# Kernel tuning notes

Measured on AMD Instinct MI355X. Metric: run time of the kernel, lower is better.

Reference implementation:

```python
import jax, jax.numpy as jnp
import numpy as np

N_HEAD = 16
D_MODEL = 1024
D_HEAD = 64
SCALE = 1.0 / D_HEAD ** 0.5
LN_EPS = 1e-5


def layer_norm(x, g, b):
    mu = jnp.mean(x, axis=-1, keepdims=True)
    var = jnp.mean(jnp.square(x - mu), axis=-1, keepdims=True)
    return (x - mu) * jax.lax.rsqrt(var + LN_EPS) * g + b


def setup_inputs() -> dict:
    key = jax.random.key(0)
    ks = jax.random.split(key, 6)
    T, B = 2048, 4
    h = jax.random.normal(ks[0], (T, B, D_MODEL), dtype=jnp.float32)
    # key-padding mask, shape (klen, bsz); True = masked
    attn_mask = jax.random.randint(ks[1], (T, B), 0, 2).astype(jnp.bool_)
    s = 1.0 / np.sqrt(D_MODEL)
    wq = jax.random.uniform(ks[2], (N_HEAD * D_HEAD, D_MODEL), minval=-s, maxval=s, dtype=jnp.float32)
    wkv = jax.random.uniform(ks[3], (2 * N_HEAD * D_HEAD, D_MODEL), minval=-s, maxval=s, dtype=jnp.float32)
    wo = jax.random.uniform(ks[4], (D_MODEL, N_HEAD * D_HEAD), minval=-s, maxval=s, dtype=jnp.float32)
    ln_g = jnp.ones((D_MODEL,), jnp.float32)
    ln_b = jnp.zeros((D_MODEL,), jnp.float32)
    return {"h": h, "attn_mask": attn_mask, "wq": wq, "wkv": wkv,
            "wo": wo, "ln_g": ln_g, "ln_b": ln_b}


def reference(h, attn_mask, wq, wkv, wo, ln_g, ln_b):
    T, B, _ = h.shape
    c = h  # mems is None
    head_q = (h @ wq.T).reshape(T, B, N_HEAD, D_HEAD)
    kv = c @ wkv.T
    head_k, head_v = jnp.split(kv, 2, axis=-1)
    head_k = head_k.reshape(T, B, N_HEAD, D_HEAD)
    head_v = head_v.reshape(T, B, N_HEAD, D_HEAD)

    # scores: [qlen, klen, bsz, n_head]
    attn_score = jnp.einsum('ibnd,jbnd->ijbn', head_q, head_k) * SCALE
    attn_score = jnp.where(attn_mask[None, :, :, None], -jnp.inf, attn_score)
    attn_prob = jax.nn.softmax(attn_score, axis=1)

    attn_vec = jnp.einsum('ijbn,jbnd->ibnd', attn_prob, head_v)
    attn_vec = attn_vec.reshape(T, B, N_HEAD * D_HEAD)
    attn_out = attn_vec @ wo.T
    # post-lnorm residual (pre_lnorm=False); gate='plus' path unused here
    return layer_norm(h + attn_out, ln_g, ln_b)
```

## Files before the change

kernel.cpp:

```cpp
#include <hip/hip_runtime.h>

#define T_LEN 2048
#define BSZ 4
#define NHEAD 16
#define DHEAD 64
#define DMODEL 1024
#define SCALE 0.125f
#define L2E_SCALE (0.125f * 1.44269504f)

typedef __bf16 bf16x8 __attribute__((ext_vector_type(8)));
typedef float f32x4 __attribute__((ext_vector_type(4)));

__device__ __forceinline__ float bf2f(unsigned short u) {
  union { unsigned int i; float f; } v; v.i = ((unsigned int)u) << 16; return v.f;
}
__device__ __forceinline__ unsigned short f2bf(float f) {
  union { float f; unsigned int i; } v; v.f = f;
  unsigned int r = v.i + 0x7fffu + ((v.i >> 16) & 1u);
  return (unsigned short)(r >> 16);
}

typedef __attribute__((address_space(1))) void* gptr_t;
typedef __attribute__((address_space(3))) void* lptr_t;

__device__ __forceinline__ void load_lds16(const void* g, void* l) {
  __builtin_amdgcn_global_load_lds((gptr_t)g, (lptr_t)l, 16, 0, 0);
}

__device__ __forceinline__ int swz16(int row, int g) {
  return row * 64 + ((g ^ (row & 7)) << 3);
}

__global__ __launch_bounds__(256) void cvt_prep(const float* __restrict__ h,
                                                const float* __restrict__ wq,
                                                const float* __restrict__ wkv,
                                                const float* __restrict__ wo,
                                                const unsigned char* __restrict__ mask,
                                                unsigned short* __restrict__ h_bf,
                                                unsigned short* __restrict__ wq_bf,
                                                unsigned short* __restrict__ wkv_bf,
                                                unsigned short* __restrict__ wo_bf,
                                                int* __restrict__ pos,
                                                int* __restrict__ nkeys) {
  const int tid = threadIdx.x;
  if (blockIdx.x < 12288) {
    const size_t E4 = (size_t)T_LEN * BSZ * DMODEL / 4;
    const size_t W4 = (size_t)NHEAD * DHEAD * DMODEL / 4;
    const size_t g = (size_t)blockIdx.x * 256 + tid;
    const float* src; unsigned short* dst; size_t off;
    if (g < E4)                { src = h;   dst = h_bf;   off = g; }
    else if (g < E4 + W4)      { src = wq;  dst = wq_bf;  off = g - E4; }
    else if (g < E4 + 3 * W4)  { src = wkv; dst = wkv_bf; off = g - E4 - W4; }
    else                       { src = wo;  dst = wo_bf;  off = g - E4 - 3 * W4; }
    const float4 v = *(const float4*)(src + off * 4);
    ushort4 o;
    o.x = f2bf(v.x); o.y = f2bf(v.y); o.z = f2bf(v.z); o.w = f2bf(v.w);
    *(ushort4*)(dst + off * 4) = o;
    return;
  }
  __shared__ int s_any;
  if (tid == 0) s_any = 0;
  __syncthreads();
  int acc = 0;
  for (int i = tid; i < T_LEN * BSZ; i += 256)
    if ((i & 3) != 0 && mask[i] != 0) acc = 1;
  if (acc) atomicOr(&s_any, 1);
  __syncthreads();
  const int mmode = s_any ? 0 : 1;
  const int wv = tid >> 6, lane = tid & 63;
  const int b = wv;
  int run = 0;
  for (int j0 = 0; j0 < T_LEN; j0 += 64) {
    const int j = j0 + lane;
    const int mval = mmode ? ((const int*)mask)[(size_t)j * BSZ + b]
                           : (int)mask[(size_t)j * BSZ + b];
    const int keep = (mval == 0) ? 1 : 0;
    int x = keep;
#pragma unroll
    for (int off = 1; off < 64; off <<= 1) {
      const int y = __shfl_up(x, off, 64);
      if (lane >= off) x += y;
    }
    pos[b * T_LEN + j] = keep ? (run + x - keep) : -1;
    run += __shfl(x, 63, 64);
  }
  if (lane == 0) nkeys[b] = run;
}

#define GEMM64_DBUF(Aptr, Bptr)                                                        \
  const int tid  = threadIdx.x;                                                        \
  const int lane = tid & 63;                                                           \
  const int wv   = tid >> 6;                                                           \
  const int wr = (wv >> 1) * 64;                                                       \
  const int wc = (wv & 1) * 64;                                                        \
  const int mi   = lane & 15;                                                          \
  const int quad = lane >> 4;                                                          \
  f32x4 acc[4][4] = {};                                                                \
  int rowc[4], colc[4];                                                                \
  _Pragma("unroll")                                                                    \
  for (int c = 0; c < 4; c++) {                                                        \
    const int s = c * 256 + tid;                                                       \
    rowc[c] = s >> 3;                                                                  \
    colc[c] = ((s & 7) ^ (rowc[c] & 7)) * 8;                                           \
  }                                                                                    \
  const int swz = mi & 7;                                                              \
  _Pragma("unroll")                                                                    \
  for (int c = 0; c < 4; c++) {                                                        \
    load_lds16(Aptr + (size_t)rowc[c] * DMODEL + colc[c], As + c * 2048 + wv * 512);   \
    load_lds16(Bptr + (size_t)rowc[c] * DMODEL + colc[c], Bs + c * 2048 + wv * 512);   \
  }                                                                                    \
  for (int k0 = 0; k0 < DMODEL; k0 += 64) {                                            \
    const int cur = (k0 >> 6) & 1;                                                     \
    const unsigned short* Asr = As + cur * 8192;                                       \
    const unsigned short* Bsr = Bs + cur * 8192;                                       \
    unsigned short* Asw = As + (1 - cur) * 8192;                                       \
    unsigned short* Bsw = Bs + (1 - cur) * 8192;                                       \
    __syncthreads();                                                                   \
    if (k0 + 64 < DMODEL) {                                                            \
      _Pragma("unroll")                                                                \
      for (int c = 0; c < 4; c++) {                                                    \
        load_lds16(Aptr + (size_t)rowc[c] * DMODEL + k0 + 64 + colc[c], Asw + c * 2048 + wv * 512); \
        load_lds16(Bptr + (size_t)rowc[c] * DMODEL + k0 + 64 + colc[c], Bsw + c * 2048 + wv * 512); \
      }                                                                                \
    }                                                                                  \
    _Pragma("unroll")                                                                  \
    for (int kq = 0; kq < 2; kq++) {                                                   \
      const int cp = ((kq * 4 + quad) ^ swz) * 8;                                      \
      bf16x8 af[4], bfr[4];                                                            \
      _Pragma("unroll")                                                                \
      for (int rt = 0; rt < 4; rt++)                                                   \
        af[rt] = *(const bf16x8*)(Asr + (wr + rt * 16 + mi) * 64 + cp);                \
      _Pragma("unroll")                                                                \
      for (int ct = 0; ct < 4; ct++)                                                   \
        bfr[ct] = *(const bf16x8*)(Bsr + (wc + ct * 16 + mi) * 64 + cp);               \
      _Pragma("unroll")                                                                \
      for (int rt = 0; rt < 4; rt++)                                                   \
        _Pragma("unroll")                                                              \
        for (int ct = 0; ct < 4; ct++)                                                 \
          acc[rt][ct] = __builtin_amdgcn_mfma_f32_16x16x32_bf16(af[rt], bfr[ct], acc[rt][ct], 0, 0, 0); \
    }                                                                                  \
  }

__global__ __launch_bounds__(256) void gemm_qkv(const unsigned short* __restrict__ A,
                                                const unsigned short* __restrict__ Wq,
                                                const unsigned short* __restrict__ Wkv,
                                                const int* __restrict__ pos,
                                                unsigned short* __restrict__ outQ,
                                                unsigned short* __restrict__ outK,
                                                unsigned short* __restrict__ outVt) {
  __shared__ alignas(16) unsigned short As[2 * 128 * 64];
  __shared__ alignas(16) unsigned short Bs[2 * 128 * 64];
  const int m0 = blockIdx.y * 128;
  const int n0 = blockIdx.x * 128;
  const unsigned short* Abase = A + (size_t)m0 * DMODEL;
  const unsigned short* Bbase = (n0 < DMODEL) ? (Wq + (size_t)n0 * DMODEL)
                                              : (Wkv + (size_t)(n0 - DMODEL) * DMODEL);
  GEMM64_DBUF(Abase, Bbase)

  const int region = n0 >> 10;
#pragma unroll
  for (int rt = 0; rt < 4; rt++) {
#pragma unroll
    for (int r = 0; r < 4; r++) {
      const int gm = m0 + wr + rt * 16 + quad * 4 + r;
      const int i = gm >> 2, b = gm & 3;
      int p = i;
      if (region > 0) p = pos[b * T_LEN + i];
      if (region > 0 && p < 0) continue;
#pragma unroll
      for (int ct = 0; ct < 4; ct++) {
        const int gn = n0 + wc + ct * 16 + mi;
        const int gnl = gn & (DMODEL - 1);
        const int hn = gnl >> 6, d = gnl & 63;
        const float v = acc[rt][ct][r];
        if (region == 0)
          outQ[(((size_t)b * NHEAD + hn) * T_LEN + i) * DHEAD + d] = f2bf(v * L2E_SCALE);
        else if (region == 1)
          outK[(((size_t)b * NHEAD + hn) * T_LEN + p) * DHEAD + d] = f2bf(v);
        else
          outVt[(((size_t)b * NHEAD + hn) * DHEAD + d) * T_LEN + p] = f2bf(v);
      }
    }
  }
}

__global__ __launch_bounds__(256) void gemm_out(const unsigned short* __restrict__ A,
                                                const unsigned short* __restrict__ Bw,
                                                unsigned short* __restrict__ outB) {
  __shared__ alignas(16) unsigned short As[2 * 128 * 64];
  __shared__ alignas(16) unsigned short Bs[2 * 128 * 64];
  const int m0 = blockIdx.y * 128;
  const int n0 = blockIdx.x * 128;
  const unsigned short* Abase = A  + (size_t)m0 * DMODEL;
  const unsigned short* Bbase = Bw + (size_t)n0 * DMODEL;
  GEMM64_DBUF(Abase, Bbase)

#pragma unroll
  for (int rt = 0; rt < 4; rt++)
#pragma unroll
    for (int ct = 0; ct < 4; ct++)
#pragma unroll
      for (int r = 0; r < 4; r++) {
        const int gm = m0 + wr + rt * 16 + quad * 4 + r;
        const int gn = n0 + wc + ct * 16 + mi;
        outB[(size_t)gm * DMODEL + gn] = f2bf(acc[rt][ct][r]);
      }
}

template<bool TAIL>
__device__ __forceinline__ void attn_chunk(int j0, int nk, int mi, int quad,
    const unsigned short* Ks, const unsigned short* Vts, unsigned short* PsW,
    const bf16x8 (&qb)[2][2], f32x4 (&oc)[2][4], float (&rs)[2]) {
  f32x4 sc[2][4] = {};
  __builtin_amdgcn_s_setprio(1);
#pragma unroll
  for (int ct = 0; ct < 4; ct++) {
    const bf16x8 kf0 = *(const bf16x8*)(Ks + swz16(ct * 16 + mi, quad));
    const bf16x8 kf1 = *(const bf16x8*)(Ks + swz16(ct * 16 + mi, 4 + quad));
#pragma unroll
    for (int g = 0; g < 2; g++) {
      sc[g][ct] = __builtin_amdgcn_mfma_f32_16x16x32_bf16(kf0, qb[g][0], sc[g][ct], 0, 0, 0);
      sc[g][ct] = __builtin_amdgcn_mfma_f32_16x16x32_bf16(kf1, qb[g][1], sc[g][ct], 0, 0, 0);
    }
  }
  __builtin_amdgcn_s_setprio(0);
#pragma unroll
  for (int g = 0; g < 2; g++)
#pragma unroll
    for (int ct = 0; ct < 4; ct++) {
#pragma unroll
      for (int r = 0; r < 4; r++) {
        float p = __builtin_amdgcn_exp2f(sc[g][ct][r]);
        if (TAIL && (j0 + ct * 16 + quad * 4 + r >= nk)) p = 0.f;
        rs[g] += p;
        sc[g][ct][r] = p;
      }
      union { float f; unsigned u; } c0, c1, c2, c3;
      c0.f = sc[g][ct][0]; c1.f = sc[g][ct][1]; c2.f = sc[g][ct][2]; c3.f = sc[g][ct][3];
      const unsigned pk0 = (c0.u >> 16) | (c1.u & 0xFFFF0000u);
      const unsigned pk1 = (c2.u >> 16) | (c3.u & 0xFFFF0000u);
      const int prow = g * 16 + mi;
      *(uint2*)(PsW + prow * 64 + (((2 * ct + (quad >> 1)) ^ (prow & 7)) << 3)
                + (quad & 1) * 4) = make_uint2(pk0, pk1);
    }
  bf16x8 pa0[2], pa1[2];
#pragma unroll
  for (int g = 0; g < 2; g++) {
    pa0[g] = *(const bf16x8*)(PsW + swz16(g * 16 + mi, quad));
    pa1[g] = *(const bf16x8*)(PsW + swz16(g * 16 + mi, 4 + quad));
  }
  __builtin_amdgcn_s_setprio(1);
#pragma unroll
  for (int ct = 0; ct < 4; ct++) {
    const bf16x8 vf0 = *(const bf16x8*)(Vts + swz16(ct * 16 + mi, quad));
    const bf16x8 vf1 = *(const bf16x8*)(Vts + swz16(ct * 16 + mi, 4 + quad));
#pragma unroll
    for (int g = 0; g < 2; g++) {
      oc[g][ct] = __builtin_amdgcn_mfma_f32_16x16x32_bf16(pa0[g], vf0, oc[g][ct], 0, 0, 0);
      oc[g][ct] = __builtin_amdgcn_mfma_f32_16x16x32_bf16(pa1[g], vf1, oc[g][ct], 0, 0, 0);
    }
  }
  __builtin_amdgcn_s_setprio(0);
}

__device__ __forceinline__ void stage_kv(const unsigned short* __restrict__ Kg,
                                         const unsigned short* __restrict__ Vtg,
                                         size_t base, int j0s, unsigned short* kb,
                                         int tid, int wv) {
#pragma unroll
  for (int u = 0; u < 2; u++) {
    const int gi = u * 256 + tid;
    const int r = gi >> 3;
    const int gs = (gi ^ r) & 7;
    load_lds16(Kg + base + (size_t)(j0s + r) * DHEAD + gs * 8,
               kb + u * 2048 + wv * 512);
    load_lds16(Vtg + base + (size_t)r * T_LEN + j0s + gs * 8,
               kb + 4096 + u * 2048 + wv * 512);
  }
}

__global__ __launch_bounds__(256, 3) void attn_mfma(const unsigned short* __restrict__ Qg,
                                                    const unsigned short* __restrict__ Kg,
                                                    const unsigned short* __restrict__ Vtg,
                                                    const int* __restrict__ nkeys,
                                                    unsigned short* __restrict__ av) {
  __shared__ alignas(16) unsigned short smem[24832];
  unsigned short* Qs = smem + 16384;
  float* Ls = (float*)(smem + 24576);

  const int tid  = threadIdx.x;
  const int lane = tid & 63;
  const int wv   = tid >> 6;
  const int mi   = lane & 15;
  const int quad = lane >> 4;
  const int bid = blockIdx.x;
  const int p   = ((bid >> 7) << 3) | (bid & 7);
  const int i0  = ((bid >> 3) & 15) * 128;
  const int b   = p >> 4;
  const int n   = p & 15;
  const size_t base = ((size_t)b * NHEAD + n) * T_LEN * DHEAD;
  const int nk = nkeys[b];
  const int nc = (nk + 63) >> 6;

  for (int it = tid; it < 1024; it += 256) {
    const int r = it >> 3, g = it & 7;
    *(uint4*)(Qs + swz16(r, g)) = *(const uint4*)(Qg + base + (size_t)(i0 + r) * DHEAD + g * 8);
  }
  if (nc > 0) stage_kv(Kg, Vtg, base, 0, smem, tid, wv);
  __syncthreads();
  bf16x8 qb[2][2];
#pragma unroll
  for (int g = 0; g < 2; g++) {
    qb[g][0] = *(const bf16x8*)(Qs + swz16(wv * 32 + g * 16 + mi, quad));
    qb[g][1] = *(const bf16x8*)(Qs + swz16(wv * 32 + g * 16 + mi, 4 + quad));
  }

  f32x4 oc[2][4] = {};
  float rs[2] = {0.f, 0.f};
  unsigned short* PsW = Qs + wv * 2048;

  for (int c = 0; c < nc; ++c) {
    if (c + 1 < nc) stage_kv(Kg, Vtg, base, (c + 1) * 64, smem + ((c + 1) & 1) * 8192, tid, wv);
    const unsigned short* Kl = smem + (c & 1) * 8192;
    const unsigned short* Vl = Kl + 4096;
    if (c == nc - 1 && (nk & 63))
      attn_chunk<true>(c * 64, nk, mi, quad, Kl, Vl, PsW, qb, oc, rs);
    else
      attn_chunk<false>(c * 64, nk, mi, quad, Kl, Vl, PsW, qb, oc, rs);
    __syncthreads();
  }

#pragma unroll
  for (int g = 0; g < 2; g++) {
    float t = rs[g];
    t += __shfl_xor(t, 16, 64);
    t += __shfl_xor(t, 32, 64);
    rs[g] = t;
  }
  if (quad == 0) { Ls[wv * 32 + mi] = rs[0]; Ls[wv * 32 + 16 + mi] = rs[1]; }
  __syncthreads();
  float linv[2][4];
#pragma unroll
  for (int g = 0; g < 2; g++)
#pragma unroll
    for (int r = 0; r < 4; r++) {
      const float l = Ls[wv * 32 + g * 16 + quad * 4 + r];
      linv[g][r] = (l > 0.f) ? (1.f / l) : 0.f;
    }
#pragma unroll
  for (int g = 0; g < 2; g++)
#pragma unroll
    for (int ct = 0; ct < 4; ct++)
#pragma unroll
      for (int r = 0; r < 4; r++) {
        const int q = i0 + wv * 32 + g * 16 + quad * 4 + r;
        const int d = ct * 16 + mi;
        av[((size_t)q * BSZ + b) * DMODEL + n * DHEAD + d] = f2bf(oc[g][ct][r] * linv[g][r]);
      }
}

__global__ __launch_bounds__(256) void ln_kernel(const float* __restrict__ h,
                                                 const unsigned short* __restrict__ ao,
                                                 const float* __restrict__ g,
                                                 const float* __restrict__ bb,
                                                 float* __restrict__ out) {
  const int tid = threadIdx.x, lane = tid & 63, wv = tid >> 6;
  const int row = blockIdx.x * 4 + wv;
  const size_t base = (size_t)row * DMODEL;
  float x[16];
  float s = 0.f, sq = 0.f;
#pragma unroll
  for (int k = 0; k < 4; k++) {
    const int c = lane * 4 + k * 256;
    const float4 hv = *(const float4*)(h + base + c);
    const ushort4 a4 = *(const ushort4*)(ao + base + c);
    x[k * 4 + 0] = hv.x + bf2f(a4.x);
    x[k * 4 + 1] = hv.y + bf2f(a4.y);
    x[k * 4 + 2] = hv.z + bf2f(a4.z);
    x[k * 4 + 3] = hv.w + bf2f(a4.w);
#pragma unroll
    for (int j = 0; j < 4; j++) { s += x[k * 4 + j]; sq += x[k * 4 + j] * x[k * 4 + j]; }
  }
#pragma unroll
  for (int off = 32; off; off >>= 1) { s += __shfl_xor(s, off, 64); sq += __shfl_xor(sq, off, 64); }
  const float mu  = s * (1.f / DMODEL);
  const float var = sq * (1.f / DMODEL) - mu * mu;
  const float inv = rsqrtf(var + 1e-5f);
#pragma unroll
  for (int k = 0; k < 4; k++) {
    const int c = lane * 4 + k * 256;
    const float4 gv = *(const float4*)(g + c);
    const float4 bv = *(const float4*)(bb + c);
    float4 o;
    o.x = (x[k * 4 + 0] - mu) * inv * gv.x + bv.x;
    o.y = (x[k * 4 + 1] - mu) * inv * gv.y + bv.y;
    o.z = (x[k * 4 + 2] - mu) * inv * gv.z + bv.z;
    o.w = (x[k * 4 + 3] - mu) * inv * gv.w + bv.w;
    *(float4*)(out + base + c) = o;
  }
}

extern "C" void kernel_launch(void* const* d_in, const int* in_sizes, int n_in,
                              void* d_out, int out_size, void* d_ws, size_t ws_size,
                              hipStream_t stream) {
  (void)in_sizes; (void)n_in; (void)out_size; (void)ws_size;
  const float* h           = (const float*)d_in[0];
  const unsigned char* msk = (const unsigned char*)d_in[1];
  const float* wq          = (const float*)d_in[2];
  const float* wkv         = (const float*)d_in[3];
  const float* wo          = (const float*)d_in[4];
  const float* lng         = (const float*)d_in[5];
  const float* lnb         = (const float*)d_in[6];
  float* out = (float*)d_out;

  const size_t E  = (size_t)T_LEN * BSZ * DMODEL;
  const size_t WQ = (size_t)NHEAD * DHEAD * DMODEL;
  char* ws = (char*)d_ws;
  int* nkeys            = (int*)ws;                       ws += 16;
  int* pos              = (int*)ws;                       ws += (size_t)BSZ * T_LEN * 4;
  unsigned short* h_bf  = (unsigned short*)ws;            ws += E * 2;
  unsigned short* wq_bf = (unsigned short*)ws;            ws += WQ * 2;
  unsigned short* wkv_bf= (unsigned short*)ws;            ws += 2 * WQ * 2;
  unsigned short* wo_bf = (unsigned short*)ws;            ws += WQ * 2;
  unsigned short* Qb    = (unsigned short*)ws;            ws += E * 2;
  unsigned short* Kb    = (unsigned short*)ws;            ws += E * 2;
  unsigned short* Vtb   = (unsigned short*)ws;            ws += E * 2;
  unsigned short* AV    = (unsigned short*)ws;            ws += E * 2;
  unsigned short* AO    = (unsigned short*)ws;

  const dim3 blk(256);
  cvt_prep<<<dim3(12289), blk, 0, stream>>>(h, wq, wkv, wo, msk,
                                            h_bf, wq_bf, wkv_bf, wo_bf, pos, nkeys);
  gemm_qkv<<<dim3(3 * DMODEL / 128, T_LEN * BSZ / 128), blk, 0, stream>>>(
      h_bf, wq_bf, wkv_bf, pos, Qb, Kb, Vtb);
  attn_mfma<<<dim3(1024), blk, 0, stream>>>(Qb, Kb, Vtb, nkeys, AV);
  gemm_out<<<dim3(DMODEL / 128, T_LEN * BSZ / 128), blk, 0, stream>>>(AV, wo_bf, AO);
  ln_kernel<<<dim3(T_LEN * BSZ / 4), blk, 0, stream>>>(h, AO, lng, lnb, out);
}
```

Baseline: 309.6 us.

## Process two 128-query tiles per attention block to reuse staged K/V

Each attention workgroup now handles 256 query rows (two 128-row tiles held in registers) instead of 128. Every K/V chunk staged into LDS is therefore used twice, halving global K/V traffic and staging overhead, and the grid shrinks from 1024 to 512 blocks. The cost is double the accumulator registers per thread, which may reduce occupancy under launch_bounds(256,3), and fewer blocks to spread across CUs. The Ls buffer is enlarged to hold row sums for both tiles.

```diff
diff --git a/kernel.cpp b/kernel.cpp
--- a/kernel.cpp
+++ b/kernel.cpp
@@ -284,7 +284,7 @@
                                                     const unsigned short* __restrict__ Vtg,
                                                     const int* __restrict__ nkeys,
                                                     unsigned short* __restrict__ av) {
-  __shared__ alignas(16) unsigned short smem[24832];
+  __shared__ alignas(16) unsigned short smem[25088];
   unsigned short* Qs = smem + 16384;
   float* Ls = (float*)(smem + 24576);
 
@@ -294,69 +294,83 @@
   const int mi   = lane & 15;
   const int quad = lane >> 4;
   const int bid = blockIdx.x;
-  const int p   = ((bid >> 7) << 3) | (bid & 7);
-  const int i0  = ((bid >> 3) & 15) * 128;
+  const int p   = ((bid >> 6) << 3) | (bid & 7);
+  const int i0  = ((bid >> 3) & 7) * 256;
   const int b   = p >> 4;
   const int n   = p & 15;
   const size_t base = ((size_t)b * NHEAD + n) * T_LEN * DHEAD;
   const int nk = nkeys[b];
   const int nc = (nk + 63) >> 6;
 
-  for (int it = tid; it < 1024; it += 256) {
-    const int r = it >> 3, g = it & 7;
-    *(uint4*)(Qs + swz16(r, g)) = *(const uint4*)(Qg + base + (size_t)(i0 + r) * DHEAD + g * 8);
-  }
   if (nc > 0) stage_kv(Kg, Vtg, base, 0, smem, tid, wv);
-  __syncthreads();
-  bf16x8 qb[2][2];
-#pragma unroll
-  for (int g = 0; g < 2; g++) {
-    qb[g][0] = *(const bf16x8*)(Qs + swz16(wv * 32 + g * 16 + mi, quad));
-    qb[g][1] = *(const bf16x8*)(Qs + swz16(wv * 32 + g * 16 + mi, 4 + quad));
-  }
-
-  f32x4 oc[2][4] = {};
-  float rs[2] = {0.f, 0.f};
+
+  bf16x8 qbA[2][2], qbB[2][2];
+#pragma unroll
+  for (int t = 0; t < 2; t++) {
+    for (int it = tid; it < 1024; it += 256) {
+      const int r = it >> 3, g = it & 7;
+      *(uint4*)(Qs + swz16(r, g)) =
+          *(const uint4*)(Qg + base + (size_t)(i0 + t * 128 + r) * DHEAD + g * 8);
+    }
+    __syncthreads();
+#pragma unroll
+    for (int g = 0; g < 2; g++) {
+      bf16x8 q0 = *(const bf16x8*)(Qs + swz16(wv * 32 + g * 16 + mi, quad));
+      bf16x8 q1 = *(const bf16x8*)(Qs + swz16(wv * 32 + g * 16 + mi, 4 + quad));
+      if (t == 0) { qbA[g][0] = q0; qbA[g][1] = q1; }
+      else        { qbB[g][0] = q0; qbB[g][1] = q1; }
+    }
+    __syncthreads();
+  }
+
+  f32x4 ocA[2][4] = {}, ocB[2][4] = {};
+  float rsA[2] = {0.f, 0.f}, rsB[2] = {0.f, 0.f};
   unsigned short* PsW = Qs + wv * 2048;
 
   for (int c = 0; c < nc; ++c) {
     if (c + 1 < nc) stage_kv(Kg, Vtg, base, (c + 1) * 64, smem + ((c + 1) & 1) * 8192, tid, wv);
     const unsigned short* Kl = smem + (c & 1) * 8192;
     const unsigned short* Vl = Kl + 4096;
-    if (c == nc - 1 && (nk & 63))
-      attn_chunk<true>(c * 64, nk, mi, quad, Kl, Vl, PsW, qb, oc, rs);
-    else
-      attn_chunk<false>(c * 64, nk, mi, quad, Kl, Vl, PsW, qb, oc, rs);
+    const int j0 = c * 64;
+    if (c == nc - 1 && (nk & 63)) {
+      attn_chunk<true>(j0, nk, mi, quad, Kl, Vl, PsW, qbA, ocA, rsA);
+      attn_chunk<true>(j0, nk, mi, quad, Kl, Vl, PsW, qbB, ocB, rsB);
+    } else {
+      attn_chunk<false>(j0, nk, mi, quad, Kl, Vl, PsW, qbA, ocA, rsA);
+      attn_chunk<false>(j0, nk, mi, quad, Kl, Vl, PsW, qbB, ocB, rsB);
+    }
     __syncthreads();
   }
 
 #pragma unroll
   for (int g = 0; g < 2; g++) {
-    float t = rs[g];
-    t += __shfl_xor(t, 16, 64);
-    t += __shfl_xor(t, 32, 64);
-    rs[g] = t;
-  }
-  if (quad == 0) { Ls[wv * 32 + mi] = rs[0]; Ls[wv * 32 + 16 + mi] = rs[1]; }
+    float tA = rsA[g], tB = rsB[g];
+    tA += __shfl_xor(tA, 16, 64); tA += __shfl_xor(tA, 32, 64);
+    tB += __shfl_xor(tB, 16, 64); tB += __shfl_xor(tB, 32, 64);
+    rsA[g] = tA; rsB[g] = tB;
+  }
+  if (quad == 0) {
+    Ls[wv * 32 + mi]        = rsA[0];  Ls[wv * 32 + 16 + mi]       = rsA[1];
+    Ls[128 + wv * 32 + mi]  = rsB[0];  Ls[128 + wv * 32 + 16 + mi] = rsB[1];
+  }
   __syncthreads();
-  float linv[2][4];
-#pragma unroll
-  for (int g = 0; g < 2; g++)
-#pragma unroll
-    for (int r = 0; r < 4; r++) {
-      const float l = Ls[wv * 32 + g * 16 + quad * 4 + r];
-      linv[g][r] = (l > 0.f) ? (1.f / l) : 0.f;
-    }
-#pragma unroll
-  for (int g = 0; g < 2; g++)
-#pragma unroll
-    for (int ct = 0; ct < 4; ct++)
+#pragma unroll
+  for (int t = 0; t < 2; t++) {
+    const f32x4 (&oc)[2][4] = t ? ocB : ocA;
+#pragma unroll
+    for (int g = 0; g < 2; g++)
 #pragma unroll
       for (int r = 0; r < 4; r++) {
-        const int q = i0 + wv * 32 + g * 16 + quad * 4 + r;
-        const int d = ct * 16 + mi;
-        av[((size_t)q * BSZ + b) * DMODEL + n * DHEAD + d] = f2bf(oc[g][ct][r] * linv[g][r]);
+        const float l = Ls[t * 128 + wv * 32 + g * 16 + quad * 4 + r];
+        const float linv = (l > 0.f) ? (1.f / l) : 0.f;
+#pragma unroll
+        for (int ct = 0; ct < 4; ct++) {
+          const int q = i0 + t * 128 + wv * 32 + g * 16 + quad * 4 + r;
+          const int d = ct * 16 + mi;
+          av[((size_t)q * BSZ + b) * DMODEL + n * DHEAD + d] = f2bf(oc[g][ct][r] * linv);
+        }
       }
+  }
 }
 
 __global__ __launch_bounds__(256) void ln_kernel(const float* __restrict__ h,
@@ -433,7 +447,7 @@
                                             h_bf, wq_bf, wkv_bf, wo_bf, pos, nkeys);
   gemm_qkv<<<dim3(3 * DMODEL / 128, T_LEN * BSZ / 128), blk, 0, stream>>>(
       h_bf, wq_bf, wkv_bf, pos, Qb, Kb, Vtb);
-  attn_mfma<<<dim3(1024), blk, 0, stream>>>(Qb, Kb, Vtb, nkeys, AV);
+  attn_mfma<<<dim3(512), blk, 0, stream>>>(Qb, Kb, Vtb, nkeys, AV);
   gemm_out<<<dim3(DMODEL / 128, T_LEN * BSZ / 128), blk, 0, stream>>>(AV, wo_bf, AO);
   ln_kernel<<<dim3(T_LEN * BSZ / 4), blk, 0, stream>>>(h, AO, lng, lnb, out);
 }
```

Result: slower. 414.5 us (+33.9%).

## Read V fragments directly from global memory and drop Q/V LDS staging

Applied to the files above, without the earlier changes.

The attention kernel no longer stages V tiles into shared memory. Each wave now loads its V MFMA fragments straight from global memory inside the PV loop, and Q fragments are loaded directly into registers instead of going through an LDS tile. This cuts LDS use so the launch bound can be raised from 3 to 4 blocks per SM for higher occupancy. The cost is that V is no longer shared across waves and is read from global/L2 on every chunk, and these loads are no longer prefetched asynchronously, so latency may appear in the MFMA loop.

```diff
diff --git a/kernel.cpp b/kernel.cpp
--- a/kernel.cpp
+++ b/kernel.cpp
@@ -209,7 +209,8 @@
 
 template<bool TAIL>
 __device__ __forceinline__ void attn_chunk(int j0, int nk, int mi, int quad,
-    const unsigned short* Ks, const unsigned short* Vts, unsigned short* PsW,
+    const unsigned short* Ks, const unsigned short* __restrict__ Vg,
+    unsigned short* PsW,
     const bf16x8 (&qb)[2][2], f32x4 (&oc)[2][4], float (&rs)[2]) {
   f32x4 sc[2][4] = {};
   __builtin_amdgcn_s_setprio(1);
@@ -252,8 +253,8 @@
   __builtin_amdgcn_s_setprio(1);
 #pragma unroll
   for (int ct = 0; ct < 4; ct++) {
-    const bf16x8 vf0 = *(const bf16x8*)(Vts + swz16(ct * 16 + mi, quad));
-    const bf16x8 vf1 = *(const bf16x8*)(Vts + swz16(ct * 16 + mi, 4 + quad));
+    const bf16x8 vf0 = *(const bf16x8*)(Vg + (size_t)(ct * 16 + mi) * T_LEN + j0 + quad * 8);
+    const bf16x8 vf1 = *(const bf16x8*)(Vg + (size_t)(ct * 16 + mi) * T_LEN + j0 + 32 + quad * 8);
 #pragma unroll
     for (int g = 0; g < 2; g++) {
       oc[g][ct] = __builtin_amdgcn_mfma_f32_16x16x32_bf16(pa0[g], vf0, oc[g][ct], 0, 0, 0);
@@ -263,10 +264,9 @@
   __builtin_amdgcn_s_setprio(0);
 }
 
-__device__ __forceinline__ void stage_kv(const unsigned short* __restrict__ Kg,
-                                         const unsigned short* __restrict__ Vtg,
-                                         size_t base, int j0s, unsigned short* kb,
-                                         int tid, int wv) {
+__device__ __forceinline__ void stage_k(const unsigned short* __restrict__ Kg,
+                                        size_t base, int j0s, unsigned short* kb,
+                                        int tid, int wv) {
 #pragma unroll
   for (int u = 0; u < 2; u++) {
     const int gi = u * 256 + tid;
@@ -274,19 +274,16 @@
     const int gs = (gi ^ r) & 7;
     load_lds16(Kg + base + (size_t)(j0s + r) * DHEAD + gs * 8,
                kb + u * 2048 + wv * 512);
-    load_lds16(Vtg + base + (size_t)r * T_LEN + j0s + gs * 8,
-               kb + 4096 + u * 2048 + wv * 512);
-  }
-}
-
-__global__ __launch_bounds__(256, 3) void attn_mfma(const unsigned short* __restrict__ Qg,
+  }
+}
+
+__global__ __launch_bounds__(256, 4) void attn_mfma(const unsigned short* __restrict__ Qg,
                                                     const unsigned short* __restrict__ Kg,
                                                     const unsigned short* __restrict__ Vtg,
                                                     const int* __restrict__ nkeys,
                                                     unsigned short* __restrict__ av) {
-  __shared__ alignas(16) unsigned short smem[24832];
-  unsigned short* Qs = smem + 16384;
-  float* Ls = (float*)(smem + 24576);
+  __shared__ alignas(16) unsigned short smem[16896];
+  float* Ls = (float*)(smem + 16384);
 
   const int tid  = threadIdx.x;
   const int lane = tid & 63;
@@ -299,34 +296,32 @@
   const int b   = p >> 4;
   const int n   = p & 15;
   const size_t base = ((size_t)b * NHEAD + n) * T_LEN * DHEAD;
+  const unsigned short* Vg = Vtg + base;
   const int nk = nkeys[b];
   const int nc = (nk + 63) >> 6;
 
-  for (int it = tid; it < 1024; it += 256) {
-    const int r = it >> 3, g = it & 7;
-    *(uint4*)(Qs + swz16(r, g)) = *(const uint4*)(Qg + base + (size_t)(i0 + r) * DHEAD + g * 8);
-  }
-  if (nc > 0) stage_kv(Kg, Vtg, base, 0, smem, tid, wv);
+  if (nc > 0) stage_k(Kg, base, 0, smem, tid, wv);
+
+  bf16x8 qb[2][2];
+#pragma unroll
+  for (int g = 0; g < 2; g++) {
+    const size_t qrow = base + (size_t)(i0 + wv * 32 + g * 16 + mi) * DHEAD;
+    qb[g][0] = *(const bf16x8*)(Qg + qrow + quad * 8);
+    qb[g][1] = *(const bf16x8*)(Qg + qrow + 32 + quad * 8);
+  }
   __syncthreads();
-  bf16x8 qb[2][2];
-#pragma unroll
-  for (int g = 0; g < 2; g++) {
-    qb[g][0] = *(const bf16x8*)(Qs + swz16(wv * 32 + g * 16 + mi, quad));
-    qb[g][1] = *(const bf16x8*)(Qs + swz16(wv * 32 + g * 16 + mi, 4 + quad));
-  }
 
   f32x4 oc[2][4] = {};
   float rs[2] = {0.f, 0.f};
-  unsigned short* PsW = Qs + wv * 2048;
+  unsigned short* PsW = smem + 8192 + wv * 2048;
 
   for (int c = 0; c < nc; ++c) {
-    if (c + 1 < nc) stage_kv(Kg, Vtg, base, (c + 1) * 64, smem + ((c + 1) & 1) * 8192, tid, wv);
-    const unsigned short* Kl = smem + (c & 1) * 8192;
-    const unsigned short* Vl = Kl + 4096;
+    if (c + 1 < nc) stage_k(Kg, base, (c + 1) * 64, smem + ((c + 1) & 1) * 4096, tid, wv);
+    const unsigned short* Kl = smem + (c & 1) * 4096;
     if (c == nc - 1 && (nk & 63))
-      attn_chunk<true>(c * 64, nk, mi, quad, Kl, Vl, PsW, qb, oc, rs);
+      attn_chunk<true>(c * 64, nk, mi, quad, Kl, Vg, PsW, qb, oc, rs);
     else
-      attn_chunk<false>(c * 64, nk, mi, quad, Kl, Vl, PsW, qb, oc, rs);
+      attn_chunk<false>(c * 64, nk, mi, quad, Kl, Vg, PsW, qb, oc, rs);
     __syncthreads();
   }
 
```

Result: slower. 352.3 us (+13.8%).
